# Optimization experiments

Measured on AMD Instinct MI355X. Metric: run time of the kernel, lower is better.

The kernel has to match this reference:

```python
import jax, jax.numpy as jnp
import numpy as np
import math

B, S, HID = 1, 2048, 2048
H, KVH, HD = 16, 4, 128
LEVEL = 256


def _rope_tables(seq_len, dim, dtype=jnp.float32):
    inv_freq = 1.0 / (10000.0 ** (np.arange(0, dim, 2, dtype=np.float32) / dim))
    ang = np.arange(seq_len, dtype=np.float32)[:, None] * inv_freq[None, :]  # [S, HD/2]
    emb = np.concatenate([ang, ang], axis=-1)  # [S, HD]
    return jnp.asarray(np.cos(emb), dtype)[None], jnp.asarray(np.sin(emb), dtype)[None]


def setup_inputs() -> dict:
    key = jax.random.key(0)
    ks = jax.random.split(key, 6)
    hidden_states = jax.random.normal(ks[0], (B, S, HID), jnp.float32)
    w_std = 1.0 / math.sqrt(HID)
    Wq = jax.random.normal(ks[1], (H * HD, HID), jnp.float32) * w_std
    Wk = jax.random.normal(ks[2], (KVH * HD, HID), jnp.float32) * w_std
    Wv = jax.random.normal(ks[3], (KVH * HD, HID), jnp.float32) * w_std
    Wo = jax.random.normal(ks[4], (HID, H * HD), jnp.float32) * w_std
    cos, sin = _rope_tables(S, HD)
    # additive causal mask [1,1,S,S]
    tri = jnp.tril(jnp.ones((S, S), jnp.bool_))
    attention_mask = jnp.where(tri, 0.0, -1e9).astype(jnp.float32)[None, None]
    return {
        "hidden_states": hidden_states,
        "Wq": Wq, "Wk": Wk, "Wv": Wv, "Wo": Wo,
        "s_q": jnp.full((1,), 0.05, jnp.float32),
        "s_k": jnp.full((1,), 0.05, jnp.float32),
        "s_v": jnp.full((1,), 0.05, jnp.float32),
        "s_attn": jnp.full((1,), 0.004, jnp.float32),
        "s_out": jnp.full((1,), 0.02, jnp.float32),
        "cos": cos, "sin": sin,
        "attention_mask": attention_mask,
    }


def _lsq(x, s, level, sym):
    # LSQ fake-quant: learned per-tensor step s, STE round, LSQ grad-scale on s.
    if sym:
        qn, qp = -level // 2, level // 2 - 1
    else:
        qn, qp = 0, level - 1
    g = 1.0 / math.sqrt(x.size * qp)          # LSQ gradient scale (static)
    s = jnp.abs(s)
    s_eff = s * g + jax.lax.stop_gradient(s - s * g)  # fwd = s, bwd grad *= g
    v = jnp.clip(x / s_eff, qn, qp)
    q = v + jax.lax.stop_gradient(jnp.round(v) - v)   # STE round
    return q * s_eff


def _rotate_half(x):
    x1, x2 = jnp.split(x, 2, axis=-1)
    return jnp.concatenate([-x2, x1], axis=-1)


def _attn_fwd(hidden_states, Wq, Wk, Wv, Wo, s_q, s_k, s_v, s_attn, s_out,
              cos, sin, attention_mask):
    b, s_len, _ = hidden_states.shape
    # projections -> [B, heads, S, HD]
    q = (hidden_states @ Wq.T).reshape(b, s_len, H, HD).transpose(0, 2, 1, 3)
    q = _lsq(q, s_q, LEVEL, sym=True)
    k = (hidden_states @ Wk.T).reshape(b, s_len, KVH, HD).transpose(0, 2, 1, 3)
    k = _lsq(k, s_k, LEVEL, sym=True)
    v = (hidden_states @ Wv.T).reshape(b, s_len, KVH, HD).transpose(0, 2, 1, 3)
    v = _lsq(v, s_v, LEVEL, sym=True)
    # RoPE (after quant, matching source order)
    c, si = cos[:, None], sin[:, None]  # [B,1,S,HD]
    q = q * c + _rotate_half(q) * si
    k = k * c + _rotate_half(k) * si
    # GQA repeat
    groups = H // KVH
    k = jnp.repeat(k, groups, axis=1)
    v = jnp.repeat(v, groups, axis=1)
    scores = jnp.einsum("bhqd,bhkd->bhqk", q, k) / math.sqrt(HD)
    scores = scores + attention_mask[:, :, :, :s_len]
    attn = jax.nn.softmax(scores.astype(jnp.float32), axis=-1).astype(q.dtype)
    attn = _lsq(attn, s_attn, LEVEL, sym=False)
    out = jnp.einsum("bhqk,bhkd->bhqd", attn, v)
    out = _lsq(out, s_out, LEVEL, sym=False)
    out = out.transpose(0, 2, 1, 3).reshape(b, s_len, H * HD)
    out = out @ Wo.T
    return out, attn


def reference(hidden_states, Wq, Wk, Wv, Wo, s_q, s_k, s_v, s_attn, s_out,
              cos, sin, attention_mask):
    return _attn_fwd(hidden_states, Wq, Wk, Wv, Wo, s_q, s_k, s_v, s_attn,
                     s_out, cos, sin, attention_mask)
```

## Files before the change

kernel.cpp:

```cpp
#include <hip/hip_runtime.h>
#include <math.h>

#define S_LEN 2048
#define HID_DIM 2048
#define NH 16
#define NKVH 4
#define HD 128
#define QD (NH*HD)
#define KD (NKVH*HD)
#define NQKV 3072

typedef _Float16 half8_t __attribute__((ext_vector_type(8)));
typedef _Float16 half4_t __attribute__((ext_vector_type(4)));
typedef float f32x4 __attribute__((ext_vector_type(4)));

#define BM 128
#define BN 128
#define BK 32

typedef const __attribute__((address_space(1))) char gas_char;
typedef __attribute__((address_space(3))) char las_char;
#define GL16(gp, lp) __builtin_amdgcn_global_load_lds((gas_char*)(gp), (las_char*)(lp), 16, 0, 0)

template<int LA, int LB, bool AF32>
__global__ __launch_bounds__(256)
void gemm_f16(const void* __restrict__ Ap, const _Float16* __restrict__ Alo,
              int lda, long long strA,
              const _Float16* __restrict__ Bhi, const _Float16* __restrict__ Blo,
              int ldb, long long strB, int divB,
              void* __restrict__ Cp, int ldc, long long strC,
              int K, float scale_c, const float* sc1, const float* sc2,
              const float* preAp,
              int qmode, const float* q1, const float* q2, const float* q3,
              int causal, int triK)
{
    int bz = blockIdx.z;
    int m0 = blockIdx.y * BM, n0 = blockIdx.x * BN;
    if (causal && n0 > m0 + (BM - 1)) return;
    int Keff = K;
    if (triK && (m0 + BM) < Keff) Keff = m0 + BM;

    const _Float16* Ahi = AF32 ? nullptr : (const _Float16*)Ap + bz * strA;
    const _Float16* AloP = (LA == 2) ? Alo + bz * strA : nullptr;
    const float* Af = AF32 ? (const float*)Ap + bz * strA : nullptr;
    const _Float16* BhiP = Bhi + (long long)(bz / divB) * strB;
    const _Float16* BloP = (LB == 2) ? Blo + (long long)(bz / divB) * strB : nullptr;
    float* Cf = (float*)Cp + bz * strC;
    _Float16* Ch = (_Float16*)Cp + bz * strC;

    float preA = 1.f;
    if (AF32) preA = 1.f / fabsf(preAp[0]);

    __shared__ _Float16 lds[(LA + LB) * 4096];
    _Float16* As0 = lds;
    _Float16* As1 = lds + 4096;
    _Float16* Bs0 = lds + LA * 4096;
    _Float16* Bs1 = lds + (LA + 1) * 4096;

    int t = threadIdx.x;
    int srow = t >> 2;
    int gsw = (srow >> 1) & 3;
    int gc = ((t & 3) ^ gsw) * 8;
    int w = t >> 6, lane = t & 63;
    int wm = (w >> 1) * 64, wn = (w & 1) * 64;
    int lr = lane & 15, lg = lane >> 4;
    int fco = ((lg ^ ((lr >> 1) & 3))) * 8;

    f32x4 acc[4][4];
    #pragma unroll
    for (int i = 0; i < 4; ++i)
        #pragma unroll
        for (int j = 0; j < 4; ++j)
            acc[i][j] = (f32x4){0.f, 0.f, 0.f, 0.f};

    for (int k0 = 0; k0 < Keff; k0 += BK) {
        f32x4 aF[2][2];
        if constexpr (AF32) {
            #pragma unroll
            for (int rep = 0; rep < 2; ++rep) {
                long long ai = (long long)(m0 + rep * 64 + srow) * lda + k0 + gc;
                aF[rep][0] = *(const f32x4*)&Af[ai];
                aF[rep][1] = *(const f32x4*)&Af[ai + 4];
            }
        }
        __syncthreads();
        #pragma unroll
        for (int rep = 0; rep < 2; ++rep) {
            int row = rep * 64 + srow;
            int lo = rep * 2048 + t * 8;
            if constexpr (!AF32) {
                long long ai = (long long)(m0 + row) * lda + k0 + gc;
                GL16(Ahi + ai, As0 + lo);
                if constexpr (LA == 2) GL16(AloP + ai, As1 + lo);
            }
            long long bi = (long long)(n0 + row) * ldb + k0 + gc;
            GL16(BhiP + bi, Bs0 + lo);
            if constexpr (LB == 2) GL16(BloP + bi, Bs1 + lo);
        }
        if constexpr (AF32) {
            #pragma unroll
            for (int rep = 0; rep < 2; ++rep) {
                half8_t h;
                #pragma unroll
                for (int e = 0; e < 4; ++e) {
                    h[e]     = (_Float16)(aF[rep][0][e] * preA);
                    h[e + 4] = (_Float16)(aF[rep][1][e] * preA);
                }
                *(half8_t*)&As0[rep * 2048 + t * 8] = h;
            }
        }
        __syncthreads();

        half8_t a0[4], b0[4];
        #pragma unroll
        for (int i = 0; i < 4; ++i) a0[i] = *(const half8_t*)&As0[(wm + i*16 + lr) * 32 + fco];
        #pragma unroll
        for (int j = 0; j < 4; ++j) b0[j] = *(const half8_t*)&Bs0[(wn + j*16 + lr) * 32 + fco];
        #pragma unroll
        for (int i = 0; i < 4; ++i)
            #pragma unroll
            for (int j = 0; j < 4; ++j)
                acc[i][j] = __builtin_amdgcn_mfma_f32_16x16x32_f16(a0[i], b0[j], acc[i][j], 0, 0, 0);
        if constexpr (LB == 2) {
            half8_t b1[4];
            #pragma unroll
            for (int j = 0; j < 4; ++j) b1[j] = *(const half8_t*)&Bs1[(wn + j*16 + lr) * 32 + fco];
            #pragma unroll
            for (int i = 0; i < 4; ++i)
                #pragma unroll
                for (int j = 0; j < 4; ++j)
                    acc[i][j] = __builtin_amdgcn_mfma_f32_16x16x32_f16(a0[i], b1[j], acc[i][j], 0, 0, 0);
        }
        if constexpr (LA == 2) {
            half8_t a1[4];
            #pragma unroll
            for (int i = 0; i < 4; ++i) a1[i] = *(const half8_t*)&As1[(wm + i*16 + lr) * 32 + fco];
            #pragma unroll
            for (int i = 0; i < 4; ++i)
                #pragma unroll
                for (int j = 0; j < 4; ++j)
                    acc[i][j] = __builtin_amdgcn_mfma_f32_16x16x32_f16(a1[i], b0[j], acc[i][j], 0, 0, 0);
        }
    }

    float se = scale_c;
    if (sc1) se *= fabsf(sc1[0]);
    if (sc2) se *= fabsf(sc2[0]);
    float sv = 1.f;
    if (qmode == 3) {
        const float* sp = (n0 < 2048) ? q1 : ((n0 < 2560) ? q2 : q3);
        sv = fabsf(sp[0]);
        qmode = 1;
    } else if (qmode) {
        sv = fabsf(q1[0]);
    }

    #pragma unroll
    for (int i = 0; i < 4; ++i)
        #pragma unroll
        for (int j = 0; j < 4; ++j)
            #pragma unroll
            for (int r = 0; r < 4; ++r) {
                long long row = m0 + wm + i * 16 + lg * 4 + r;
                long long col = n0 + wn + j * 16 + lr;
                float v = acc[i][j][r] * se;
                if (qmode == 0) {
                    Cf[row * (long long)ldc + col] = v;
                } else if (qmode == 1) {
                    float u = rintf(fminf(fmaxf(v / sv, -128.f), 127.f));
                    Ch[row * (long long)ldc + col] = (_Float16)u;
                } else {
                    float u = rintf(fminf(fmaxf(v / sv, 0.f), 255.f));
                    Ch[row * (long long)ldc + col] = (_Float16)u;
                }
            }
}

__global__ void split_f16(const float* __restrict__ in, _Float16* __restrict__ hi,
                          _Float16* __restrict__ lo, int n4)
{
    int i = blockIdx.x * 256 + threadIdx.x;
    if (i >= n4) return;
    f32x4 v = ((const f32x4*)in)[i];
    half4_t h, l;
    #pragma unroll
    for (int e = 0; e < 4; ++e) {
        h[e] = (_Float16)v[e];
        l[e] = (_Float16)(v[e] - (float)h[e]);
    }
    ((half4_t*)hi)[i] = h;
    ((half4_t*)lo)[i] = l;
}

__global__ void rope_f16(const _Float16* __restrict__ codes, int ldc_, int colOff,
                         const float* __restrict__ cosT,
                         const float* __restrict__ sinT,
                         _Float16* __restrict__ ohi, _Float16* __restrict__ olo, int nh)
{
    long long idx = (long long)blockIdx.x * 256 + threadIdx.x;
    int d = idx & (HD - 1);
    long long tt = idx >> 7;
    int h = (int)(tt % nh);
    int s = (int)(tt / nh);
    long long base = (long long)s * ldc_ + colOff + h * HD;
    float x = (float)codes[base + d];
    float other = (d < 64) ? -(float)codes[base + d + 64] : (float)codes[base + d - 64];
    float o = x * cosT[s * HD + d] + other * sinT[s * HD + d];
    _Float16 hf = (_Float16)o;
    long long oi = ((long long)h * S_LEN + s) * HD + d;
    ohi[oi] = hf;
    olo[oi] = (_Float16)(o - (float)hf);
}

__global__ __launch_bounds__(256)
void transpose_vf16(const _Float16* __restrict__ in, _Float16* __restrict__ outp)
{
    __shared__ _Float16 tile[64][72];
    int s0 = blockIdx.x * 64, d0 = blockIdx.y * 64, h = blockIdx.z;
    int t = threadIdx.x;
    int rr = t >> 4, cc = (t & 15) * 4;
    #pragma unroll
    for (int r = 0; r < 4; ++r) {
        half4_t v = *(const half4_t*)&in[(long long)(s0 + rr + 16*r) * NQKV + 2560 + h * HD + d0 + cc];
        *(half4_t*)&tile[rr + 16*r][cc] = v;
    }
    __syncthreads();
    #pragma unroll
    for (int r = 0; r < 4; ++r) {
        int dr = rr + 16 * r;
        half4_t o = { tile[cc+0][dr], tile[cc+1][dr], tile[cc+2][dr], tile[cc+3][dr] };
        *(half4_t*)&outp[((long long)h * HD + d0 + dr) * S_LEN + s0 + cc] = o;
    }
}

__global__ __launch_bounds__(256)
void softmax_quant(float* __restrict__ attn, const float* __restrict__ sPtr)
{
    int row = blockIdx.x;
    int q = row & (S_LEN - 1);
    float* p = attn + (long long)row * S_LEN;
    int n = q + 1;
    int tid = threadIdx.x;

    __shared__ float buf[S_LEN];
    __shared__ float swm[4];
    __shared__ float sws[4];

    float mx = -INFINITY;
    for (int i = tid; i < n; i += 256) {
        float v = p[i];
        buf[i] = v;
        mx = fmaxf(mx, v);
    }
    #pragma unroll
    for (int o = 32; o; o >>= 1) mx = fmaxf(mx, __shfl_xor(mx, o));
    if ((tid & 63) == 0) swm[tid >> 6] = mx;
    __syncthreads();
    mx = fmaxf(fmaxf(swm[0], swm[1]), fmaxf(swm[2], swm[3]));

    float lsum = 0.f;
    for (int i = tid; i < n; i += 256) {
        float e = expf(buf[i] - mx);
        buf[i] = e;
        lsum += e;
    }
    #pragma unroll
    for (int o = 32; o; o >>= 1) lsum += __shfl_xor(lsum, o);
    if ((tid & 63) == 0) sws[tid >> 6] = lsum;
    __syncthreads();
    float tot = sws[0] + sws[1] + sws[2] + sws[3];

    float sa = fabsf(sPtr[0]);
    for (int i = tid; i < n; i += 256) {
        float pr = buf[i] / tot;
        float t = fminf(fmaxf(pr / sa, 0.f), 255.f);
        p[i] = rintf(t) * sa;
    }
    for (int i = tid; i < S_LEN; i += 256)
        if (i >= n) p[i] = 0.f;
}

extern "C" void kernel_launch(void* const* d_in, const int* in_sizes, int n_in,
                              void* d_out, int out_size, void* d_ws, size_t ws_size,
                              hipStream_t stream)
{
    const float* hs    = (const float*)d_in[0];
    const float* Wq    = (const float*)d_in[1];
    const float* Wk    = (const float*)d_in[2];
    const float* Wv    = (const float*)d_in[3];
    const float* Wo    = (const float*)d_in[4];
    const float* s_q   = (const float*)d_in[5];
    const float* s_k   = (const float*)d_in[6];
    const float* s_v   = (const float*)d_in[7];
    const float* s_at  = (const float*)d_in[8];
    const float* s_out = (const float*)d_in[9];
    const float* cosT  = (const float*)d_in[10];
    const float* sinT  = (const float*)d_in[11];

    float* out  = (float*)d_out;
    float* attn = out + (long long)S_LEN * HID_DIM;

    const long long M1 = 1LL * 1024 * 1024;
    const long long M4 = 4LL * M1;
    const long long M6 = 6LL * M1;

    _Float16* wsh   = (_Float16*)d_ws;
    _Float16* qr_hi = wsh;
    _Float16* qr_lo = qr_hi + M4;
    _Float16* kr_hi = qr_lo + M4;
    _Float16* kr_lo = kr_hi + M1;
    _Float16* vT    = kr_lo + M1;
    _Float16* ao    = vT + M1;
    _Float16* Wo_hi = ao + M4;
    _Float16* Wo_lo = Wo_hi + M4;

    _Float16* sc      = (_Float16*)attn;
    _Float16* hs_hi   = sc;
    _Float16* hs_lo   = hs_hi + M4;
    _Float16* Whi     = hs_lo + M4;
    _Float16* Wlo     = Whi + M6;
    _Float16* qkvcode = Wlo + M6;

    dim3 blk(256);
    const float iscale = 0.08838834764831845f;

    split_f16<<<4096, blk, 0, stream>>>(hs, hs_hi, hs_lo, 1024*1024);
    split_f16<<<4096, blk, 0, stream>>>(Wq, Whi, Wlo, 1024*1024);
    split_f16<<<1024, blk, 0, stream>>>(Wk, Whi + 2048LL*2048, Wlo + 2048LL*2048, 256*1024);
    split_f16<<<1024, blk, 0, stream>>>(Wv, Whi + 2560LL*2048, Wlo + 2560LL*2048, 256*1024);
    split_f16<<<4096, blk, 0, stream>>>(Wo, Wo_hi, Wo_lo, 1024*1024);

    gemm_f16<2,2,false><<<dim3(NQKV/BN, S_LEN/BM, 1), blk, 0, stream>>>(
        hs_hi, hs_lo, HID_DIM, 0, Whi, Wlo, HID_DIM, 0, 1,
        qkvcode, NQKV, 0, HID_DIM, 1.f, nullptr, nullptr, nullptr,
        3, s_q, s_k, s_v, 0, 0);

    rope_f16<<<(NH*S_LEN*HD)/256, blk, 0, stream>>>(qkvcode, NQKV, 0, cosT, sinT, qr_hi, qr_lo, NH);
    rope_f16<<<(NKVH*S_LEN*HD)/256, blk, 0, stream>>>(qkvcode, NQKV, 2048, cosT, sinT, kr_hi, kr_lo, NKVH);
    transpose_vf16<<<dim3(S_LEN/64, HD/64, NKVH), blk, 0, stream>>>(qkvcode, vT);

    gemm_f16<2,2,false><<<dim3(S_LEN/BN, S_LEN/BM, NH), blk, 0, stream>>>(
        qr_hi, qr_lo, HD, (long long)S_LEN*HD,
        kr_hi, kr_lo, HD, (long long)S_LEN*HD, NH/NKVH,
        attn, S_LEN, (long long)S_LEN*S_LEN,
        HD, iscale, s_q, s_k, nullptr, 0, nullptr, nullptr, nullptr, 1, 0);

    softmax_quant<<<NH*S_LEN, blk, 0, stream>>>(attn, s_at);

    gemm_f16<1,1,true><<<dim3(1, S_LEN/BM, NH), blk, 0, stream>>>(
        attn, nullptr, S_LEN, (long long)S_LEN*S_LEN,
        vT, nullptr, S_LEN, (long long)HD*S_LEN, NH/NKVH,
        ao, QD, HD,
        S_LEN, 1.f, s_at, s_v, s_at, 2, s_out, nullptr, nullptr, 0, 1);

    gemm_f16<1,2,false><<<dim3(HID_DIM/BN, S_LEN/BM, 1), blk, 0, stream>>>(
        ao, nullptr, QD, 0, Wo_hi, Wo_lo, QD, 0, 1,
        out, HID_DIM, 0, QD, 1.f, s_out, nullptr, nullptr,
        0, nullptr, nullptr, nullptr, 0, 0);
}
```

Before: 493.1 us.

## Fuse softmax-quant into PV GEMM using partial max/sum from the score GEMM

Result: slower. 551.4 us (+11.8%).

```diff
diff --git a/kernel.cpp b/kernel.cpp
--- a/kernel.cpp
+++ b/kernel.cpp
@@ -22,7 +22,7 @@
 typedef __attribute__((address_space(3))) char las_char;
 #define GL16(gp, lp) __builtin_amdgcn_global_load_lds((gas_char*)(gp), (las_char*)(lp), 16, 0, 0)
 
-template<int LA, int LB, bool AF32>
+template<int LA, int LB, bool AF32, bool PSM>
 __global__ __launch_bounds__(256)
 void gemm_f16(const void* __restrict__ Ap, const _Float16* __restrict__ Alo,
               int lda, long long strA,
@@ -32,7 +32,7 @@
               int K, float scale_c, const float* sc1, const float* sc2,
               const float* preAp,
               int qmode, const float* q1, const float* q2, const float* q3,
-              int causal, int triK)
+              int causal, int triK, float* __restrict__ pml)
 {
     int bz = blockIdx.z;
     int m0 = blockIdx.y * BM, n0 = blockIdx.x * BN;
@@ -174,6 +174,152 @@
                     Ch[row * (long long)ldc + col] = (_Float16)u;
                 }
             }
+
+    if constexpr (PSM) {
+        int cb64 = (n0 + wn) >> 6;
+        #pragma unroll
+        for (int i = 0; i < 4; ++i)
+            #pragma unroll
+            for (int r = 0; r < 4; ++r) {
+                int row = m0 + wm + i * 16 + lg * 4 + r;
+                float vv[4];
+                float mloc = -INFINITY;
+                #pragma unroll
+                for (int j = 0; j < 4; ++j) {
+                    int col = n0 + wn + j * 16 + lr;
+                    float v = acc[i][j][r] * se;
+                    vv[j] = (col <= row) ? v : -INFINITY;
+                    mloc = fmaxf(mloc, vv[j]);
+                }
+                #pragma unroll
+                for (int o = 1; o < 16; o <<= 1) mloc = fmaxf(mloc, __shfl_xor(mloc, o));
+                float sloc = 0.f;
+                #pragma unroll
+                for (int j = 0; j < 4; ++j) sloc += expf(vv[j] - mloc);
+                #pragma unroll
+                for (int o = 1; o < 16; o <<= 1) sloc += __shfl_xor(sloc, o);
+                if (lr == 0) {
+                    long long idx = (((long long)bz * S_LEN + row) * 32 + cb64) * 2;
+                    pml[idx] = mloc;
+                    pml[idx + 1] = sloc;
+                }
+            }
+    }
+}
+
+__global__ __launch_bounds__(256)
+void reduce_ml(const float* __restrict__ pml, float* __restrict__ fml)
+{
+    int id = blockIdx.x * 256 + threadIdx.x;
+    int r = id & (S_LEN - 1);
+    int nb = (r >> 6) + 1;
+    float m = -INFINITY, l = 0.f;
+    const float* p = pml + (long long)id * 64;
+    for (int cb = 0; cb < nb; ++cb) {
+        float mp = p[cb * 2], lp = p[cb * 2 + 1];
+        float mn = fmaxf(m, mp);
+        l = l * expf(m - mn) + lp * expf(mp - mn);
+        m = mn;
+    }
+    fml[id * 2] = m;
+    fml[id * 2 + 1] = l;
+}
+
+__global__ __launch_bounds__(256)
+void fused_pv(float* __restrict__ attn, const _Float16* __restrict__ vT,
+              const float* __restrict__ fml, _Float16* __restrict__ ao,
+              const float* s_at_p, const float* s_v_p, const float* s_out_p)
+{
+    int rb = blockIdx.x;
+    int h = blockIdx.y;
+    int m0 = rb * 64;
+    float* S = attn + (long long)h * S_LEN * S_LEN;
+    const _Float16* V = vT + (long long)(h >> 2) * HD * S_LEN;
+
+    float sa = fabsf(s_at_p[0]);
+    float seo = sa * fabsf(s_v_p[0]) / fabsf(s_out_p[0]);
+
+    __shared__ _Float16 Bs[128 * 32];
+    __shared__ float ml[64][2];
+
+    int t = threadIdx.x;
+    int w = t >> 6, lane = t & 63;
+    int lr = lane & 15, lg = lane >> 4;
+    int wr0 = m0 + w * 16;
+    int row = wr0 + lr;
+
+    if (t < 64) {
+        ml[t][0] = fml[((long long)h * S_LEN + m0 + t) * 2];
+        ml[t][1] = fml[((long long)h * S_LEN + m0 + t) * 2 + 1];
+    }
+    __syncthreads();
+    float mrow = ml[w * 16 + lr][0];
+    float lrow = ml[w * 16 + lr][1];
+
+    int srow = t >> 2;
+    int gsw = (srow >> 1) & 3;
+    int gc = ((t & 3) ^ gsw) * 8;
+    int fco = ((lg ^ ((lr >> 1) & 3))) * 8;
+
+    f32x4 acc[8];
+    #pragma unroll
+    for (int j = 0; j < 8; ++j) acc[j] = (f32x4){0.f, 0.f, 0.f, 0.f};
+
+    int kmax = m0 + 64;
+    for (int k0 = 0; k0 < kmax; k0 += 32) {
+        __syncthreads();
+        #pragma unroll
+        for (int rep = 0; rep < 2; ++rep)
+            GL16(&V[(long long)(rep * 64 + srow) * S_LEN + k0 + gc], &Bs[rep * 2048 + t * 8]);
+
+        int c0 = k0 + lg * 8;
+        long long sbase = (long long)row * S_LEN + c0;
+        f32x4 s1 = *(const f32x4*)&S[sbase];
+        f32x4 s2 = *(const f32x4*)&S[sbase + 4];
+        half8_t af;
+        f32x4 o1, o2;
+        #pragma unroll
+        for (int e = 0; e < 8; ++e) {
+            float sv_ = (e < 4) ? s1[e] : s2[e - 4];
+            float u = 0.f;
+            if (c0 + e <= row) {
+                float p = expf(sv_ - mrow) / lrow;
+                u = rintf(fminf(fmaxf(p / sa, 0.f), 255.f));
+            }
+            af[e] = (_Float16)u;
+            if (e < 4) o1[e] = u * sa; else o2[e - 4] = u * sa;
+        }
+        *(f32x4*)&S[sbase] = o1;
+        *(f32x4*)&S[sbase + 4] = o2;
+
+        __syncthreads();
+        if (k0 <= wr0 + 15) {
+            half8_t bf[8];
+            #pragma unroll
+            for (int j = 0; j < 8; ++j)
+                bf[j] = *(const half8_t*)&Bs[(j * 16 + lr) * 32 + fco];
+            #pragma unroll
+            for (int j = 0; j < 8; ++j)
+                acc[j] = __builtin_amdgcn_mfma_f32_16x16x32_f16(af, bf[j], acc[j], 0, 0, 0);
+        }
+    }
+
+    {
+        int rr = t >> 2, l4 = (t & 3) * 4;
+        f32x4 z = (f32x4){0.f, 0.f, 0.f, 0.f};
+        for (int cc = kmax + l4; cc < S_LEN; cc += 16)
+            *(f32x4*)&S[(long long)(m0 + rr) * S_LEN + cc] = z;
+    }
+
+    #pragma unroll
+    for (int j = 0; j < 8; ++j)
+        #pragma unroll
+        for (int r = 0; r < 4; ++r) {
+            int orow = wr0 + lg * 4 + r;
+            int d = j * 16 + lr;
+            float u = rintf(fminf(fmaxf(acc[j][r] * seo, 0.f), 255.f));
+            ao[(long long)orow * QD + h * HD + d] = (_Float16)u;
+        }
 }
 
 __global__ void split_f16(const float* __restrict__ in, _Float16* __restrict__ hi,
@@ -233,53 +379,6 @@
     }
 }
 
-__global__ __launch_bounds__(256)
-void softmax_quant(float* __restrict__ attn, const float* __restrict__ sPtr)
-{
-    int row = blockIdx.x;
-    int q = row & (S_LEN - 1);
-    float* p = attn + (long long)row * S_LEN;
-    int n = q + 1;
-    int tid = threadIdx.x;
-
-    __shared__ float buf[S_LEN];
-    __shared__ float swm[4];
-    __shared__ float sws[4];
-
-    float mx = -INFINITY;
-    for (int i = tid; i < n; i += 256) {
-        float v = p[i];
-        buf[i] = v;
-        mx = fmaxf(mx, v);
-    }
-    #pragma unroll
-    for (int o = 32; o; o >>= 1) mx = fmaxf(mx, __shfl_xor(mx, o));
-    if ((tid & 63) == 0) swm[tid >> 6] = mx;
-    __syncthreads();
-    mx = fmaxf(fmaxf(swm[0], swm[1]), fmaxf(swm[2], swm[3]));
-
-    float lsum = 0.f;
-    for (int i = tid; i < n; i += 256) {
-        float e = expf(buf[i] - mx);
-        buf[i] = e;
-        lsum += e;
-    }
-    #pragma unroll
-    for (int o = 32; o; o >>= 1) lsum += __shfl_xor(lsum, o);
-    if ((tid & 63) == 0) sws[tid >> 6] = lsum;
-    __syncthreads();
-    float tot = sws[0] + sws[1] + sws[2] + sws[3];
-
-    float sa = fabsf(sPtr[0]);
-    for (int i = tid; i < n; i += 256) {
-        float pr = buf[i] / tot;
-        float t = fminf(fmaxf(pr / sa, 0.f), 255.f);
-        p[i] = rintf(t) * sa;
-    }
-    for (int i = tid; i < S_LEN; i += 256)
-        if (i >= n) p[i] = 0.f;
-}
-
 extern "C" void kernel_launch(void* const* d_in, const int* in_sizes, int n_in,
                               void* d_out, int out_size, void* d_ws, size_t ws_size,
                               hipStream_t stream)
@@ -321,6 +420,9 @@
     _Float16* Wlo     = Whi + M6;
     _Float16* qkvcode = Wlo + M6;
 
+    float* pml = out;
+    float* fml = out + 2LL * 1024 * 1024;
+
     dim3 blk(256);
     const float iscale = 0.08838834764831845f;
 
@@ -330,31 +432,28 @@
     split_f16<<<1024, blk, 0, stream>>>(Wv, Whi + 2560LL*2048, Wlo + 2560LL*2048, 256*1024);
     split_f16<<<4096, blk, 0, stream>>>(Wo, Wo_hi, Wo_lo, 1024*1024);
 
-    gemm_f16<2,2,false><<<dim3(NQKV/BN, S_LEN/BM, 1), blk, 0, stream>>>(
+    gemm_f16<2,2,false,false><<<dim3(NQKV/BN, S_LEN/BM, 1), blk, 0, stream>>>(
         hs_hi, hs_lo, HID_DIM, 0, Whi, Wlo, HID_DIM, 0, 1,
         qkvcode, NQKV, 0, HID_DIM, 1.f, nullptr, nullptr, nullptr,
-        3, s_q, s_k, s_v, 0, 0);
+        3, s_q, s_k, s_v, 0, 0, nullptr);
 
     rope_f16<<<(NH*S_LEN*HD)/256, blk, 0, stream>>>(qkvcode, NQKV, 0, cosT, sinT, qr_hi, qr_lo, NH);
     rope_f16<<<(NKVH*S_LEN*HD)/256, blk, 0, stream>>>(qkvcode, NQKV, 2048, cosT, sinT, kr_hi, kr_lo, NKVH);
     transpose_vf16<<<dim3(S_LEN/64, HD/64, NKVH), blk, 0, stream>>>(qkvcode, vT);
 
-    gemm_f16<2,2,false><<<dim3(S_LEN/BN, S_LEN/BM, NH), blk, 0, stream>>>(
+    gemm_f16<2,2,false,true><<<dim3(S_LEN/BN, S_LEN/BM, NH), blk, 0, stream>>>(
         qr_hi, qr_lo, HD, (long long)S_LEN*HD,
         kr_hi, kr_lo, HD, (long long)S_LEN*HD, NH/NKVH,
         attn, S_LEN, (long long)S_LEN*S_LEN,
-        HD, iscale, s_q, s_k, nullptr, 0, nullptr, nullptr, nullptr, 1, 0);
-
-    softmax_quant<<<NH*S_LEN, blk, 0, stream>>>(attn, s_at);
-
-    gemm_f16<1,1,true><<<dim3(1, S_LEN/BM, NH), blk, 0, stream>>>(
-        attn, nullptr, S_LEN, (long long)S_LEN*S_LEN,
-        vT, nullptr, S_LEN, (long long)HD*S_LEN, NH/NKVH,
-        ao, QD, HD,
-        S_LEN, 1.f, s_at, s_v, s_at, 2, s_out, nullptr, nullptr, 0, 1);
-
-    gemm_f16<1,2,false><<<dim3(HID_DIM/BN, S_LEN/BM, 1), blk, 0, stream>>>(
+        HD, iscale, s_q, s_k, nullptr, 0, nullptr, nullptr, nullptr, 1, 0, pml);
+
+    reduce_ml<<<(NH*S_LEN)/256, blk, 0, stream>>>(pml, fml);
+
+    fused_pv<<<dim3(S_LEN/64, NH), blk, 0, stream>>>(
+        attn, vT, fml, ao, s_at, s_v, s_out);
+
+    gemm_f16<1,2,false,false><<<dim3(HID_DIM/BN, S_LEN/BM, 1), blk, 0, stream>>>(
         ao, nullptr, QD, 0, Wo_hi, Wo_lo, QD, 0, 1,
         out, HID_DIM, 0, QD, 1.f, s_out, nullptr, nullptr,
-        0, nullptr, nullptr, nullptr, 0, 0);
-}
+        0, nullptr, nullptr, nullptr, 0, 0, nullptr);
+}
```
